# Performance work log

Hardware: AMD Instinct MI355X
Metric: run time of the kernel (lower is better)

Reference implementation:

```python
import jax, jax.numpy as jnp
import numpy as np

B, XDIM, YDIM = 131072, 128, 512


def setup_inputs() -> dict:
    key = jax.random.key(0)
    k1, k2, k3, k4 = jax.random.split(key, 4)
    return {
        "mean": jax.random.normal(k1, (B, XDIM), dtype=jnp.float32),
        "logvar": jax.random.normal(k2, (B, XDIM), dtype=jnp.float32),
        "W": jax.random.normal(k3, (YDIM, XDIM), dtype=jnp.float32) * 0.1,
        "b": jax.random.normal(k4, (YDIM,), dtype=jnp.float32) * 0.1,
    }


def reference(mean, logvar, W, b):
    # mean branch: standard Linear  y = mean @ W^T + b
    mean_out = jnp.einsum("bx,yx->by", mean, W) + b  # [B, ydim]
    # variance branch: v_i = sum_j C_ij^2 * exp(logvar_j)
    # (equivalent to diag(C S S^T C^T) with S = diag(exp(0.5*logvar)))
    v = jnp.einsum("yx,bx->by", W * W, jnp.exp(logvar))  # [B, ydim]
    return mean_out, jnp.log(v)
```

## Files before the change

kernel.cpp:

```cpp
#include <hip/hip_runtime.h>
#include <hip/hip_bf16.h>

#define XDIM 128
#define YDIM 512

typedef __bf16 bf16x8 __attribute__((ext_vector_type(8)));
typedef float  floatx4 __attribute__((ext_vector_type(4)));

__global__ __launch_bounds__(256, 2)
void decoder_mfma_kernel(const float* __restrict__ mean,
                         const float* __restrict__ logvar,
                         const float* __restrict__ W,
                         const float* __restrict__ bias,
                         float* __restrict__ out_mean,
                         float* __restrict__ out_logv)
{
    const int tid   = threadIdx.x;
    const int lane  = tid & 63;
    const int wv    = tid >> 6;
    const int laneM = lane & 15;
    const int laneK = (lane >> 4) * 8;

    const int row_base = blockIdx.x * 32;
    const int col_base = wv * 128;

    bf16x8 aM[2][4], aV[2][4];
#pragma unroll
    for (int rt = 0; rt < 2; ++rt) {
        const int r = row_base + rt * 16 + laneM;
        const float* mrow = mean   + (size_t)r * XDIM + laneK;
        const float* lrow = logvar + (size_t)r * XDIM + laneK;
#pragma unroll
        for (int ks = 0; ks < 4; ++ks) {
            floatx4 m0 = *(const floatx4*)(mrow + ks * 32);
            floatx4 m1 = *(const floatx4*)(mrow + ks * 32 + 4);
            floatx4 l0 = *(const floatx4*)(lrow + ks * 32);
            floatx4 l1 = *(const floatx4*)(lrow + ks * 32 + 4);
            bf16x8 am, av;
#pragma unroll
            for (int j = 0; j < 4; ++j) {
                am[j]     = (__bf16)m0[j];
                am[j + 4] = (__bf16)m1[j];
                av[j]     = (__bf16)__expf(l0[j]);
                av[j + 4] = (__bf16)__expf(l1[j]);
            }
            aM[rt][ks] = am;
            aV[rt][ks] = av;
        }
    }

    floatx4 accM[2][8], accV[2][8];
#pragma unroll
    for (int rt = 0; rt < 2; ++rt)
#pragma unroll
        for (int ct = 0; ct < 8; ++ct) {
            accM[rt][ct] = (floatx4){0.f, 0.f, 0.f, 0.f};
            accV[rt][ct] = (floatx4){0.f, 0.f, 0.f, 0.f};
        }

#pragma unroll
    for (int ks = 0; ks < 4; ++ks) {
#pragma unroll
        for (int ct = 0; ct < 8; ++ct) {
            const float* wrow = W + (size_t)(col_base + ct * 16 + laneM) * XDIM
                                  + ks * 32 + laneK;
            floatx4 w0 = *(const floatx4*)(wrow);
            floatx4 w1 = *(const floatx4*)(wrow + 4);
            bf16x8 bw, bs;
#pragma unroll
            for (int j = 0; j < 4; ++j) {
                bw[j]     = (__bf16)w0[j];
                bw[j + 4] = (__bf16)w1[j];
                bs[j]     = (__bf16)(w0[j] * w0[j]);
                bs[j + 4] = (__bf16)(w1[j] * w1[j]);
            }
#pragma unroll
            for (int rt = 0; rt < 2; ++rt) {
                accM[rt][ct] = __builtin_amdgcn_mfma_f32_16x16x32_bf16(
                                   aM[rt][ks], bw, accM[rt][ct], 0, 0, 0);
                accV[rt][ct] = __builtin_amdgcn_mfma_f32_16x16x32_bf16(
                                   aV[rt][ks], bs, accV[rt][ct], 0, 0, 0);
            }
        }
    }

#pragma unroll
    for (int ct = 0; ct < 8; ++ct) {
        const int col = col_base + ct * 16 + laneM;
        const float bv = bias[col];
#pragma unroll
        for (int rt = 0; rt < 2; ++rt) {
            const int r0 = row_base + rt * 16 + (lane >> 4) * 4;
#pragma unroll
            for (int i = 0; i < 4; ++i) {
                out_mean[(size_t)(r0 + i) * YDIM + col] = accM[rt][ct][i] + bv;
                out_logv[(size_t)(r0 + i) * YDIM + col] = __logf(accV[rt][ct][i]);
            }
        }
    }
}

extern "C" void kernel_launch(void* const* d_in, const int* in_sizes, int n_in,
                              void* d_out, int out_size, void* d_ws, size_t ws_size,
                              hipStream_t stream)
{
    const float* mean   = (const float*)d_in[0];
    const float* logvar = (const float*)d_in[1];
    const float* W      = (const float*)d_in[2];
    const float* bias   = (const float*)d_in[3];

    const int batch = in_sizes[0] / XDIM;
    float* out_mean = (float*)d_out;
    float* out_logv = (float*)d_out + (size_t)batch * YDIM;

    dim3 grid(batch / 32);
    dim3 block(256);
    hipLaunchKernelGGL(decoder_mfma_kernel, grid, block, 0, stream,
                       mean, logvar, W, bias, out_mean, out_logv);
}
```

Measured before the change: 781.1 us.

## Precast W to bf16 in workspace and transpose MFMA operands for vector stores

Adds a prep kernel that converts W and W squared to bf16 once per call in the workspace, so the main kernel loads bf16x8 directly instead of converting fp32 per block. The main kernel swaps MFMA operand roles so each lane owns four consecutive output columns, enabling 16-byte nontemporal stores and a vector bias load. It also splits the column work into two halves to cut live accumulators and raises the occupancy hint to 3. This adds an extra launch and depends on the workspace being large enough.

```diff
diff --git a/kernel.cpp b/kernel.cpp
--- a/kernel.cpp
+++ b/kernel.cpp
@@ -6,6 +6,122 @@
 
 typedef __bf16 bf16x8 __attribute__((ext_vector_type(8)));
 typedef float  floatx4 __attribute__((ext_vector_type(4)));
+
+__global__ __launch_bounds__(256)
+void prep_w_kernel(const float* __restrict__ W,
+                   __bf16* __restrict__ Wb,
+                   __bf16* __restrict__ W2b)
+{
+    const int t = blockIdx.x * 256 + threadIdx.x;
+    const float* src = W + (size_t)t * 8;
+    floatx4 a = *(const floatx4*)(src);
+    floatx4 c = *(const floatx4*)(src + 4);
+    bf16x8 w, w2;
+#pragma unroll
+    for (int j = 0; j < 4; ++j) {
+        w[j]      = (__bf16)a[j];
+        w[j + 4]  = (__bf16)c[j];
+        w2[j]     = (__bf16)(a[j] * a[j]);
+        w2[j + 4] = (__bf16)(c[j] * c[j]);
+    }
+    *(bf16x8*)(Wb  + (size_t)t * 8) = w;
+    *(bf16x8*)(W2b + (size_t)t * 8) = w2;
+}
+
+__global__ __launch_bounds__(256, 3)
+void decoder_mfma_v2(const float* __restrict__ mean,
+                     const float* __restrict__ logvar,
+                     const __bf16* __restrict__ Wb,
+                     const __bf16* __restrict__ W2b,
+                     const float* __restrict__ bias,
+                     float* __restrict__ out_mean,
+                     float* __restrict__ out_logv)
+{
+    const int tid   = threadIdx.x;
+    const int lane  = tid & 63;
+    const int wv    = tid >> 6;
+    const int laneM = lane & 15;
+    const int laneG = lane >> 4;
+    const int laneK = laneG * 8;
+
+    const int row_base = blockIdx.x * 32;
+    const int col_base = wv * 128;
+
+    bf16x8 bM[2][4], bV[2][4];
+#pragma unroll
+    for (int rt = 0; rt < 2; ++rt) {
+        const int r = row_base + rt * 16 + laneM;
+        const float* mrow = mean   + (size_t)r * XDIM + laneK;
+        const float* lrow = logvar + (size_t)r * XDIM + laneK;
+#pragma unroll
+        for (int ks = 0; ks < 4; ++ks) {
+            floatx4 m0 = *(const floatx4*)(mrow + ks * 32);
+            floatx4 m1 = *(const floatx4*)(mrow + ks * 32 + 4);
+            floatx4 l0 = *(const floatx4*)(lrow + ks * 32);
+            floatx4 l1 = *(const floatx4*)(lrow + ks * 32 + 4);
+            bf16x8 fm, fv;
+#pragma unroll
+            for (int j = 0; j < 4; ++j) {
+                fm[j]     = (__bf16)m0[j];
+                fm[j + 4] = (__bf16)m1[j];
+                fv[j]     = (__bf16)__expf(l0[j]);
+                fv[j + 4] = (__bf16)__expf(l1[j]);
+            }
+            bM[rt][ks] = fm;
+            bV[rt][ks] = fv;
+        }
+    }
+
+#pragma unroll
+    for (int h = 0; h < 2; ++h) {
+        floatx4 accM[2][4], accV[2][4];
+#pragma unroll
+        for (int rt = 0; rt < 2; ++rt)
+#pragma unroll
+            for (int ct = 0; ct < 4; ++ct) {
+                accM[rt][ct] = (floatx4){0.f, 0.f, 0.f, 0.f};
+                accV[rt][ct] = (floatx4){0.f, 0.f, 0.f, 0.f};
+            }
+
+#pragma unroll
+        for (int ks = 0; ks < 4; ++ks) {
+#pragma unroll
+            for (int ct = 0; ct < 4; ++ct) {
+                const size_t off =
+                    (size_t)(col_base + h * 64 + ct * 16 + laneM) * XDIM
+                    + ks * 32 + laneK;
+                bf16x8 aw = *(const bf16x8*)(Wb  + off);
+                bf16x8 as = *(const bf16x8*)(W2b + off);
+#pragma unroll
+                for (int rt = 0; rt < 2; ++rt) {
+                    accM[rt][ct] = __builtin_amdgcn_mfma_f32_16x16x32_bf16(
+                                       aw, bM[rt][ks], accM[rt][ct], 0, 0, 0);
+                    accV[rt][ct] = __builtin_amdgcn_mfma_f32_16x16x32_bf16(
+                                       as, bV[rt][ks], accV[rt][ct], 0, 0, 0);
+                }
+            }
+        }
+
+#pragma unroll
+        for (int ct = 0; ct < 4; ++ct) {
+            const int ybase = col_base + h * 64 + ct * 16 + laneG * 4;
+            const floatx4 bv = *(const floatx4*)(bias + ybase);
+#pragma unroll
+            for (int rt = 0; rt < 2; ++rt) {
+                const int r = row_base + rt * 16 + laneM;
+                floatx4 om = accM[rt][ct] + bv;
+                floatx4 ol;
+#pragma unroll
+                for (int i = 0; i < 4; ++i)
+                    ol[i] = __logf(accV[rt][ct][i]);
+                __builtin_nontemporal_store(
+                    om, (floatx4*)(out_mean + (size_t)r * YDIM + ybase));
+                __builtin_nontemporal_store(
+                    ol, (floatx4*)(out_logv + (size_t)r * YDIM + ybase));
+            }
+        }
+    }
+}
 
 __global__ __launch_bounds__(256, 2)
 void decoder_mfma_kernel(const float* __restrict__ mean,
@@ -113,8 +229,17 @@
     float* out_mean = (float*)d_out;
     float* out_logv = (float*)d_out + (size_t)batch * YDIM;
 
-    dim3 grid(batch / 32);
-    dim3 block(256);
-    hipLaunchKernelGGL(decoder_mfma_kernel, grid, block, 0, stream,
-                       mean, logvar, W, bias, out_mean, out_logv);
-}
+    const size_t ws_need = (size_t)YDIM * XDIM * sizeof(__bf16) * 2;
+
+    if (d_ws != nullptr && ws_size >= ws_need) {
+        __bf16* Wb  = (__bf16*)d_ws;
+        __bf16* W2b = Wb + (size_t)YDIM * XDIM;
+        hipLaunchKernelGGL(prep_w_kernel, dim3(32), dim3(256), 0, stream,
+                           W, Wb, W2b);
+        hipLaunchKernelGGL(decoder_mfma_v2, dim3(batch / 32), dim3(256), 0, stream,
+                           mean, logvar, Wb, W2b, bias, out_mean, out_logv);
+    } else {
+        hipLaunchKernelGGL(decoder_mfma_kernel, dim3(batch / 32), dim3(256), 0, stream,
+                           mean, logvar, W, bias, out_mean, out_logv);
+    }
+}
```

Result: no change. 775.0 us (-0.8%).
